# Optimization experiments

Measured on AMD Instinct MI355X. Metric: run time of the kernel, lower is better.

The kernel has to match this reference:

```python
import jax, jax.numpy as jnp
import numpy as np

B, L, HID = 4, 4096, 1024
H, D = 16, 64  # num_heads, head_dim


def setup_inputs() -> dict:
    key = jax.random.key(0)
    ks = jax.random.split(key, 5)
    s = 1.0 / np.sqrt(HID)
    mk = lambda k: jax.random.uniform(k, (HID, HID), minval=-s, maxval=s, dtype=jnp.float32)
    return {
        "x": jax.random.normal(ks[0], (B, L, HID), dtype=jnp.float32),
        "Wq": mk(ks[1]), "bq": jnp.zeros((HID,), jnp.float32),
        "Wk": mk(ks[2]), "bk": jnp.zeros((HID,), jnp.float32),
        "Wv": mk(ks[3]), "bv": jnp.zeros((HID,), jnp.float32),
        "Wo": mk(ks[4]), "bo": jnp.zeros((HID,), jnp.float32),
    }


def reference(x, Wq, bq, Wk, bk, Wv, bv, Wo, bo):
    Bx, Lx, _ = x.shape
    # projections (weights stored [in, out])
    q = (x @ Wq + bq).reshape(Bx, Lx, H, D)
    k = (x @ Wk + bk).reshape(Bx, Lx, H, D)
    v = (x @ Wv + bv).reshape(Bx, Lx, H, D)
    # Single window (L <= window_size): torch matmul batches over (B, L) and
    # contracts head_dim -> per-token head-to-head scores [B, L, H, H].
    scores = jnp.einsum('blhd,bled->blhe', q, k) / np.sqrt(D).astype(np.float32)
    probs = jax.nn.softmax(scores, axis=-1)
    out = jnp.einsum('blhe,bled->blhd', probs, v).reshape(Bx, Lx, HID)
    return out @ Wo + bo
```

## Files before the change

kernel.cpp:

```cpp
#include <hip/hip_runtime.h>
#include <stdint.h>


typedef __attribute__((ext_vector_type(8))) short short8;
typedef __attribute__((ext_vector_type(4))) float floatx4;
typedef __attribute__((address_space(1))) unsigned int gu32;
typedef __attribute__((address_space(3))) unsigned int lu32;

#define HID 1024
#define MTOK 16384
#define WELEM (HID * HID)
#define XELEM (MTOK * HID)

#define SBAR() __builtin_amdgcn_s_barrier()
#define WAITLGKM() do { asm volatile("s_waitcnt lgkmcnt(0)" ::: "memory"); \
                        __builtin_amdgcn_sched_barrier(0); } while (0)

__device__ __forceinline__ unsigned short f2bf(float f) {
  union { float f; uint32_t u; } v; v.f = f;
  uint32_t u = v.u;
  u += 0x7fffu + ((u >> 16) & 1u);
  return (unsigned short)(u >> 16);
}

__global__ __launch_bounds__(256) void cvt_x_kernel(const float* __restrict__ x,
                                                    unsigned short* __restrict__ xb) {
  const int idx = blockIdx.x * 256 + threadIdx.x;
  float4 v = ((const float4*)x)[idx];
  ushort4 o;
  o.x = f2bf(v.x); o.y = f2bf(v.y); o.z = f2bf(v.z); o.w = f2bf(v.w);
  ((ushort4*)xb)[idx] = o;
}

__global__ __launch_bounds__(256) void cvt_w_kernel(const float* __restrict__ W0,
                                                    const float* __restrict__ W1,
                                                    const float* __restrict__ W2,
                                                    const float* __restrict__ W3,
                                                    unsigned short* __restrict__ WT) {
  const float* W = (blockIdx.z == 0) ? W0 : (blockIdx.z == 1) ? W1
                   : (blockIdx.z == 2) ? W2 : W3;
  unsigned short* out = WT + (size_t)blockIdx.z * WELEM;
  __shared__ float tile[64][65];
  const int t = threadIdx.x;
  const int n0 = blockIdx.x * 64, k0 = blockIdx.y * 64;
#pragma unroll
  for (int i = 0; i < 4; i++) {
    const int row = i * 16 + (t >> 4);
    const int col = (t & 15) * 4;
    float4 v = *(const float4*)&W[(size_t)(k0 + row) * HID + n0 + col];
    tile[row][col] = v.x; tile[row][col + 1] = v.y;
    tile[row][col + 2] = v.z; tile[row][col + 3] = v.w;
  }
  __syncthreads();
#pragma unroll
  for (int i = 0; i < 4; i++) {
    const int n = i * 16 + (t >> 4);
    const int k = (t & 15) * 4;
    ushort4 o;
    o.x = f2bf(tile[k][n]);     o.y = f2bf(tile[k + 1][n]);
    o.z = f2bf(tile[k + 2][n]); o.w = f2bf(tile[k + 3][n]);
    *(ushort4*)&out[(size_t)(n0 + n) * HID + k0 + k] = o;
  }
}

template <bool QKV>
__global__ __launch_bounds__(512, 2) void gemm256(
    const unsigned short* __restrict__ A,
    const unsigned short* __restrict__ BTb,
    const float* __restrict__ b0, const float* __restrict__ b1,
    const float* __restrict__ b2,
    void* __restrict__ Cv)
{
  __shared__ short8 smem_[131072 / 16];
  char* smem = (char*)smem_;

  const int bid = blockIdx.x;
  const int xcd = bid & 7;
  const int j = bid >> 3;
  const int nb = j >> 3;
  const int mb = xcd * 8 + (j & 7);
  const int m0 = mb * 256;
  const int n0 = nb * 256;

  const unsigned short* BT = QKV ? BTb : (BTb + (size_t)3 * WELEM);

  const int t_ = threadIdx.x;
  const int wv = t_ >> 6, lane = t_ & 63;
  const int quad = lane >> 4, r16 = lane & 15;
  const int wm = wv >> 2, wn = wv & 3;

  const int srow = wv * 16 + (lane >> 2);
  const int scol = ((lane & 3) ^ ((lane >> 3) & 3)) * 8;
  const unsigned short* Ag = A  + (size_t)(m0 + srow) * HID + scol;
  const unsigned short* Bg = BT + (size_t)(n0 + srow) * HID + scol;

  const int qsw = (quad ^ ((r16 >> 1) & 3)) << 4;
  const char* Ard = smem + wm * 16384 + r16 * 64 + qsw;
  const char* Brd = smem + 32768 + (wn >> 1) * 16384 + ((wn & 1) * 64 + r16) * 64 + qsw;

  floatx4 acc[8][4] = {};

  auto stageA = [&](int h, int tt) {
    const unsigned short* s = Ag + (size_t)h * 128 * HID + tt * 64;
    char* d = smem + ((tt & 1) << 16) + h * 16384 + wv * 1024;
    __builtin_amdgcn_global_load_lds((const gu32*)s,        (lu32*)d,          16, 0, 0);
    __builtin_amdgcn_global_load_lds((const gu32*)(s + 32), (lu32*)(d + 8192), 16, 0, 0);
  };
  auto stageB = [&](int h, int tt) {
    const unsigned short* s = Bg + (size_t)h * 128 * HID + tt * 64;
    char* d = smem + ((tt & 1) << 16) + 32768 + h * 16384 + wv * 1024;
    __builtin_amdgcn_global_load_lds((const gu32*)s,        (lu32*)d,          16, 0, 0);
    __builtin_amdgcn_global_load_lds((const gu32*)(s + 32), (lu32*)(d + 8192), 16, 0, 0);
  };

  stageA(0, 0); stageA(1, 0); stageB(0, 0); stageB(1, 0);
  stageB(0, 1); stageA(0, 1);
  asm volatile("s_waitcnt vmcnt(4)" ::: "memory");
  SBAR();

  short8 a[4][2], b01[2][2], b23[2][2];
  const int NT = HID / 64;

  for (int t = 0; t < NT; ++t) {
    const int bufb = (t & 1) << 16;

#pragma unroll
    for (int ks = 0; ks < 2; ++ks) {
#pragma unroll
      for (int mi = 0; mi < 4; ++mi)
        a[mi][ks] = *(const short8*)(Ard + bufb + ks * 8192 + mi * 1024);
#pragma unroll
      for (int ni = 0; ni < 2; ++ni)
        b01[ni][ks] = *(const short8*)(Brd + bufb + ks * 8192 + ni * 1024);
    }
    if (t + 1 < NT) stageA(1, t + 1);
    SBAR(); WAITLGKM();
    __builtin_amdgcn_s_setprio(1);
#pragma unroll
    for (int ks = 0; ks < 2; ++ks)
#pragma unroll
      for (int mi = 0; mi < 4; ++mi)
#pragma unroll
        for (int ni = 0; ni < 2; ++ni)
          acc[mi][ni] = __builtin_amdgcn_mfma_f32_16x16x32_bf16(a[mi][ks], b01[ni][ks], acc[mi][ni], 0, 0, 0);
    __builtin_amdgcn_s_setprio(0);
    SBAR();

#pragma unroll
    for (int ks = 0; ks < 2; ++ks)
#pragma unroll
      for (int ni = 0; ni < 2; ++ni)
        b23[ni][ks] = *(const short8*)(Brd + bufb + ks * 8192 + (2 + ni) * 1024);
    if (t + 1 < NT) stageB(1, t + 1);
    SBAR(); WAITLGKM();
    __builtin_amdgcn_s_setprio(1);
#pragma unroll
    for (int ks = 0; ks < 2; ++ks)
#pragma unroll
      for (int mi = 0; mi < 4; ++mi)
#pragma unroll
        for (int ni = 0; ni < 2; ++ni)
          acc[mi][2 + ni] = __builtin_amdgcn_mfma_f32_16x16x32_bf16(a[mi][ks], b23[ni][ks], acc[mi][2 + ni], 0, 0, 0);
    __builtin_amdgcn_s_setprio(0);
    SBAR();

#pragma unroll
    for (int ks = 0; ks < 2; ++ks) {
#pragma unroll
      for (int mi = 0; mi < 4; ++mi)
        a[mi][ks] = *(const short8*)(Ard + bufb + ks * 8192 + (4 + mi) * 1024);
#pragma unroll
      for (int ni = 0; ni < 2; ++ni)
        b01[ni][ks] = *(const short8*)(Brd + bufb + ks * 8192 + ni * 1024);
    }
    SBAR(); WAITLGKM();
    __builtin_amdgcn_s_setprio(1);
#pragma unroll
    for (int ks = 0; ks < 2; ++ks)
#pragma unroll
      for (int mi = 0; mi < 4; ++mi)
#pragma unroll
        for (int ni = 0; ni < 2; ++ni)
          acc[4 + mi][ni] = __builtin_amdgcn_mfma_f32_16x16x32_bf16(a[mi][ks], b01[ni][ks], acc[4 + mi][ni], 0, 0, 0);
    __builtin_amdgcn_s_setprio(0);
    SBAR();

    if (t + 2 < NT) { stageB(0, t + 2); stageA(0, t + 2); }
    SBAR();
    __builtin_amdgcn_s_setprio(1);
#pragma unroll
    for (int ks = 0; ks < 2; ++ks)
#pragma unroll
      for (int mi = 0; mi < 4; ++mi)
#pragma unroll
        for (int ni = 0; ni < 2; ++ni)
          acc[4 + mi][2 + ni] = __builtin_amdgcn_mfma_f32_16x16x32_bf16(a[mi][ks], b23[ni][ks], acc[4 + mi][2 + ni], 0, 0, 0);
    __builtin_amdgcn_s_setprio(0);
    if (t + 2 < NT)      { asm volatile("s_waitcnt vmcnt(4)" ::: "memory"); }
    else if (t + 1 < NT) { asm volatile("s_waitcnt vmcnt(0)" ::: "memory"); }
    SBAR();
  }

  const int cb = QKV ? (n0 & 1023) : n0;
  const int zX = QKV ? (n0 >> 10) : 0;
  const float* bias = QKV ? ((zX == 0) ? b0 : ((zX == 1) ? b1 : b2)) : b0;

  float bvv[4];
#pragma unroll
  for (int ni = 0; ni < 4; ++ni) bvv[ni] = bias[cb + wn * 64 + ni * 16 + r16];

  const int row0 = m0 + wm * 128 + quad * 4;
  unsigned short* outb = (unsigned short*)Cv + (size_t)zX * XELEM;
  float* outf = (float*)Cv;
#pragma unroll
  for (int mi = 0; mi < 8; ++mi) {
#pragma unroll
    for (int rr = 0; rr < 4; ++rr) {
      const size_t roff = (size_t)(row0 + mi * 16 + rr) * HID + cb + wn * 64 + r16;
#pragma unroll
      for (int ni = 0; ni < 4; ++ni) {
        const float val = acc[mi][ni][rr] + bvv[ni];
        if constexpr (QKV) outb[roff + ni * 16] = f2bf(val);
        else               outf[roff + ni * 16] = val;
      }
    }
  }
}

__global__ __launch_bounds__(256) void attn_kernel(const unsigned short* qkv,
                                                   unsigned short* attn) {
  __shared__ unsigned short vls[4][1056];
  __shared__ unsigned short pls[4][16 * 24];

  const int t = threadIdx.x;
  const int wv = t >> 6, lane = t & 63;
  const int quad = lane >> 4, r16 = lane & 15;
  const size_t base = ((size_t)blockIdx.x * 4 + wv) * HID;
  const unsigned short* qp = qkv + base;
  const unsigned short* kp = qkv + (size_t)XELEM + base;
  const unsigned short* vp = qkv + 2 * (size_t)XELEM + base;

  __builtin_amdgcn_global_load_lds((const gu32*)(vp + lane * 8),       (lu32*)&vls[wv][0],   16, 0, 0);
  __builtin_amdgcn_global_load_lds((const gu32*)(vp + 512 + lane * 8), (lu32*)&vls[wv][528], 16, 0, 0);

  short8 qf0 = *(const short8*)(qp + r16 * 64 + quad * 8);
  short8 qf1 = *(const short8*)(qp + r16 * 64 + quad * 8 + 32);
  short8 kf0 = *(const short8*)(kp + r16 * 64 + quad * 8);
  short8 kf1 = *(const short8*)(kp + r16 * 64 + quad * 8 + 32);

  floatx4 sc = {0.f, 0.f, 0.f, 0.f};
  sc = __builtin_amdgcn_mfma_f32_16x16x32_bf16(qf0, kf0, sc, 0, 0, 0);
  sc = __builtin_amdgcn_mfma_f32_16x16x32_bf16(qf1, kf1, sc, 0, 0, 0);

#pragma unroll
  for (int rr = 0; rr < 4; rr++) {
    float s = sc[rr] * 0.125f;
    float m = s;
#pragma unroll
    for (int off = 1; off < 16; off <<= 1) m = fmaxf(m, __shfl_xor(m, off));
    float ex = __expf(s - m);
    float sum = ex;
#pragma unroll
    for (int off = 1; off < 16; off <<= 1) sum += __shfl_xor(sum, off);
    pls[wv][(quad * 4 + rr) * 24 + r16] = f2bf(ex / sum);
  }

  __syncthreads();

  const short8 zero8 = {0, 0, 0, 0, 0, 0, 0, 0};
  short8 af = zero8;
  short8 bf[4] = {zero8, zero8, zero8, zero8};
  if (quad < 2) {
    af = *(const short8*)&pls[wv][r16 * 24 + quad * 8];
#pragma unroll
    for (int c = 0; c < 4; c++)
#pragma unroll
      for (int jj = 0; jj < 8; jj++)
        bf[c][jj] = (short)vls[wv][quad * 528 + jj * 64 + c * 16 + r16];
  }

  floatx4 ov[4];
#pragma unroll
  for (int c = 0; c < 4; c++) {
    floatx4 z = {0.f, 0.f, 0.f, 0.f};
    ov[c] = __builtin_amdgcn_mfma_f32_16x16x32_bf16(af, bf[c], z, 0, 0, 0);
  }

#pragma unroll
  for (int rr = 0; rr < 4; rr++)
#pragma unroll
    for (int c = 0; c < 4; c++)
      attn[base + (size_t)(quad * 4 + rr) * 64 + c * 16 + r16] = f2bf(ov[c][rr]);
}

extern "C" void kernel_launch(void* const* d_in, const int* in_sizes, int n_in,
                              void* d_out, int out_size, void* d_ws, size_t ws_size,
                              hipStream_t stream) {
  const float* x  = (const float*)d_in[0];
  const float* Wq = (const float*)d_in[1];
  const float* bq = (const float*)d_in[2];
  const float* Wk = (const float*)d_in[3];
  const float* bk = (const float*)d_in[4];
  const float* Wv = (const float*)d_in[5];
  const float* bv = (const float*)d_in[6];
  const float* Wo = (const float*)d_in[7];
  const float* bo = (const float*)d_in[8];

  char* ws = (char*)d_ws;
  unsigned short* xb  = (unsigned short*)ws;
  unsigned short* wt  = (unsigned short*)(ws + (size_t)XELEM * 2);
  unsigned short* qkv = wt + 4 * (size_t)WELEM;

  cvt_x_kernel<<<XELEM / 1024, 256, 0, stream>>>(x, xb);
  cvt_w_kernel<<<dim3(16, 16, 4), 256, 0, stream>>>(Wq, Wk, Wv, Wo, wt);
  gemm256<true><<<768, 512, 0, stream>>>(xb, wt, bq, bk, bv, (void*)qkv);
  attn_kernel<<<4096, 256, 0, stream>>>(qkv, qkv);
  gemm256<false><<<256, 512, 0, stream>>>(qkv, wt, bo, bo, bo, d_out);
}
```

Baseline: 302.5 us.

## Loop each QKV GEMM block over Q,K,V weights and pipeline B-fragment reads across tiles

The QKV GEMM now launches 256 blocks, each computing the same 256x256 output tile for all three projections in sequence. A block reloads the next weight's first tiles while it writes out the current epilogue. Inside the K loop, the B-fragment registers for columns 0-1 are double-buffered, so the next tile's fragments are read during the current tile. The stage ordering and vmcnt waits are reworked to match. This trims LDS reads and hides latency at the cost of more registers. It also drops the grid from 768 to 256 blocks, which cuts parallelism and may leave CUs underused.

```diff
diff --git a/kernel.cpp b/kernel.cpp
--- a/kernel.cpp
+++ b/kernel.cpp
@@ -15,6 +15,8 @@
 #define SBAR() __builtin_amdgcn_s_barrier()
 #define WAITLGKM() do { asm volatile("s_waitcnt lgkmcnt(0)" ::: "memory"); \
                         __builtin_amdgcn_sched_barrier(0); } while (0)
+#define VMCNT(n) do { asm volatile("s_waitcnt vmcnt(" #n ")" ::: "memory"); \
+                      __builtin_amdgcn_sched_barrier(0); } while (0)
 
 __device__ __forceinline__ unsigned short f2bf(float f) {
   union { float f; uint32_t u; } v; v.f = f;
@@ -74,15 +76,16 @@
   __shared__ short8 smem_[131072 / 16];
   char* smem = (char*)smem_;
 
+  constexpr int R = QKV ? 3 : 1;
   const int bid = blockIdx.x;
   const int xcd = bid & 7;
   const int j = bid >> 3;
-  const int nb = j >> 3;
+  const int nb0 = j >> 3;
   const int mb = xcd * 8 + (j & 7);
   const int m0 = mb * 256;
-  const int n0 = nb * 256;
-
-  const unsigned short* BT = QKV ? BTb : (BTb + (size_t)3 * WELEM);
+  const int cb = nb0 * 256;
+
+  const unsigned short* BT0 = QKV ? BTb : (BTb + (size_t)3 * WELEM);
 
   const int t_ = threadIdx.x;
   const int wv = t_ >> 6, lane = t_ & 63;
@@ -91,8 +94,8 @@
 
   const int srow = wv * 16 + (lane >> 2);
   const int scol = ((lane & 3) ^ ((lane >> 3) & 3)) * 8;
-  const unsigned short* Ag = A  + (size_t)(m0 + srow) * HID + scol;
-  const unsigned short* Bg = BT + (size_t)(n0 + srow) * HID + scol;
+  const unsigned short* Ag = A + (size_t)(m0 + srow) * HID + scol;
+  const unsigned short* Bg = BT0 + (size_t)(cb + srow) * HID + scol;
 
   const int qsw = (quad ^ ((r16 >> 1) & 3)) << 4;
   const char* Ard = smem + wm * 16384 + r16 * 64 + qsw;
@@ -113,26 +116,36 @@
     __builtin_amdgcn_global_load_lds((const gu32*)(s + 32), (lu32*)(d + 8192), 16, 0, 0);
   };
 
-  stageA(0, 0); stageA(1, 0); stageB(0, 0); stageB(1, 0);
-  stageB(0, 1); stageA(0, 1);
-  asm volatile("s_waitcnt vmcnt(4)" ::: "memory");
-  SBAR();
-
-  short8 a[4][2], b01[2][2], b23[2][2];
   const int NT = HID / 64;
 
-  for (int t = 0; t < NT; ++t) {
-    const int bufb = (t & 1) << 16;
-
-#pragma unroll
-    for (int ks = 0; ks < 2; ++ks) {
+  short8 a[4][2];
+  short8 b23[2][2];
+  short8 bA[2][2], bB[2][2];
+
+  auto TILE = [&](int t, int bufb, int othb, short8 (&bc)[2][2], short8 (&bn)[2][2]) {
+#pragma unroll
+    for (int ks = 0; ks < 2; ++ks)
 #pragma unroll
       for (int mi = 0; mi < 4; ++mi)
         a[mi][ks] = *(const short8*)(Ard + bufb + ks * 8192 + mi * 1024);
+    if (t + 1 < NT) stageA(0, t + 1);
+    SBAR(); WAITLGKM();
+    __builtin_amdgcn_s_setprio(1);
+#pragma unroll
+    for (int ks = 0; ks < 2; ++ks)
+#pragma unroll
+      for (int mi = 0; mi < 4; ++mi)
+#pragma unroll
+        for (int ni = 0; ni < 2; ++ni)
+          acc[mi][ni] = __builtin_amdgcn_mfma_f32_16x16x32_bf16(a[mi][ks], bc[ni][ks], acc[mi][ni], 0, 0, 0);
+    __builtin_amdgcn_s_setprio(0);
+    SBAR();
+
+#pragma unroll
+    for (int ks = 0; ks < 2; ++ks)
 #pragma unroll
       for (int ni = 0; ni < 2; ++ni)
-        b01[ni][ks] = *(const short8*)(Brd + bufb + ks * 8192 + ni * 1024);
-    }
+        b23[ni][ks] = *(const short8*)(Brd + bufb + ks * 8192 + (2 + ni) * 1024);
     if (t + 1 < NT) stageA(1, t + 1);
     SBAR(); WAITLGKM();
     __builtin_amdgcn_s_setprio(1);
@@ -142,16 +155,16 @@
       for (int mi = 0; mi < 4; ++mi)
 #pragma unroll
         for (int ni = 0; ni < 2; ++ni)
-          acc[mi][ni] = __builtin_amdgcn_mfma_f32_16x16x32_bf16(a[mi][ks], b01[ni][ks], acc[mi][ni], 0, 0, 0);
+          acc[mi][2 + ni] = __builtin_amdgcn_mfma_f32_16x16x32_bf16(a[mi][ks], b23[ni][ks], acc[mi][2 + ni], 0, 0, 0);
     __builtin_amdgcn_s_setprio(0);
     SBAR();
 
 #pragma unroll
     for (int ks = 0; ks < 2; ++ks)
 #pragma unroll
-      for (int ni = 0; ni < 2; ++ni)
-        b23[ni][ks] = *(const short8*)(Brd + bufb + ks * 8192 + (2 + ni) * 1024);
-    if (t + 1 < NT) stageB(1, t + 1);
+      for (int mi = 0; mi < 4; ++mi)
+        a[mi][ks] = *(const short8*)(Ard + bufb + ks * 8192 + (4 + mi) * 1024);
+    if (t + 2 < NT) stageB(0, t + 2);
     SBAR(); WAITLGKM();
     __builtin_amdgcn_s_setprio(1);
 #pragma unroll
@@ -160,69 +173,94 @@
       for (int mi = 0; mi < 4; ++mi)
 #pragma unroll
         for (int ni = 0; ni < 2; ++ni)
-          acc[mi][2 + ni] = __builtin_amdgcn_mfma_f32_16x16x32_bf16(a[mi][ks], b23[ni][ks], acc[mi][2 + ni], 0, 0, 0);
-    __builtin_amdgcn_s_setprio(0);
-    SBAR();
-
-#pragma unroll
-    for (int ks = 0; ks < 2; ++ks) {
-#pragma unroll
-      for (int mi = 0; mi < 4; ++mi)
-        a[mi][ks] = *(const short8*)(Ard + bufb + ks * 8192 + (4 + mi) * 1024);
-#pragma unroll
-      for (int ni = 0; ni < 2; ++ni)
-        b01[ni][ks] = *(const short8*)(Brd + bufb + ks * 8192 + ni * 1024);
-    }
-    SBAR(); WAITLGKM();
-    __builtin_amdgcn_s_setprio(1);
-#pragma unroll
-    for (int ks = 0; ks < 2; ++ks)
-#pragma unroll
-      for (int mi = 0; mi < 4; ++mi)
-#pragma unroll
-        for (int ni = 0; ni < 2; ++ni)
-          acc[4 + mi][ni] = __builtin_amdgcn_mfma_f32_16x16x32_bf16(a[mi][ks], b01[ni][ks], acc[4 + mi][ni], 0, 0, 0);
-    __builtin_amdgcn_s_setprio(0);
-    SBAR();
-
-    if (t + 2 < NT) { stageB(0, t + 2); stageA(0, t + 2); }
-    SBAR();
-    __builtin_amdgcn_s_setprio(1);
-#pragma unroll
-    for (int ks = 0; ks < 2; ++ks)
-#pragma unroll
-      for (int mi = 0; mi < 4; ++mi)
-#pragma unroll
-        for (int ni = 0; ni < 2; ++ni)
           acc[4 + mi][2 + ni] = __builtin_amdgcn_mfma_f32_16x16x32_bf16(a[mi][ks], b23[ni][ks], acc[4 + mi][2 + ni], 0, 0, 0);
     __builtin_amdgcn_s_setprio(0);
-    if (t + 2 < NT)      { asm volatile("s_waitcnt vmcnt(4)" ::: "memory"); }
-    else if (t + 1 < NT) { asm volatile("s_waitcnt vmcnt(0)" ::: "memory"); }
-    SBAR();
-  }
-
-  const int cb = QKV ? (n0 & 1023) : n0;
-  const int zX = QKV ? (n0 >> 10) : 0;
-  const float* bias = QKV ? ((zX == 0) ? b0 : ((zX == 1) ? b1 : b2)) : b0;
-
-  float bvv[4];
-#pragma unroll
-  for (int ni = 0; ni < 4; ++ni) bvv[ni] = bias[cb + wn * 64 + ni * 16 + r16];
-
-  const int row0 = m0 + wm * 128 + quad * 4;
-  unsigned short* outb = (unsigned short*)Cv + (size_t)zX * XELEM;
-  float* outf = (float*)Cv;
-#pragma unroll
-  for (int mi = 0; mi < 8; ++mi) {
-#pragma unroll
-    for (int rr = 0; rr < 4; ++rr) {
-      const size_t roff = (size_t)(row0 + mi * 16 + rr) * HID + cb + wn * 64 + r16;
-#pragma unroll
-      for (int ni = 0; ni < 4; ++ni) {
-        const float val = acc[mi][ni][rr] + bvv[ni];
-        if constexpr (QKV) outb[roff + ni * 16] = f2bf(val);
-        else               outf[roff + ni * 16] = val;
+    if (t + 2 < NT)      { VMCNT(6); }
+    else if (t + 1 < NT) { VMCNT(4); }
+    SBAR();
+
+    if (t + 1 < NT) {
+#pragma unroll
+      for (int ks = 0; ks < 2; ++ks)
+#pragma unroll
+        for (int ni = 0; ni < 2; ++ni)
+          bn[ni][ks] = *(const short8*)(Brd + othb + ks * 8192 + ni * 1024);
+    }
+    if (t + 2 < NT) stageB(1, t + 2);
+    SBAR();
+    __builtin_amdgcn_s_setprio(1);
+#pragma unroll
+    for (int ks = 0; ks < 2; ++ks)
+#pragma unroll
+      for (int mi = 0; mi < 4; ++mi)
+#pragma unroll
+        for (int ni = 0; ni < 2; ++ni)
+          acc[4 + mi][ni] = __builtin_amdgcn_mfma_f32_16x16x32_bf16(a[mi][ks], bc[ni][ks], acc[4 + mi][ni], 0, 0, 0);
+    __builtin_amdgcn_s_setprio(0);
+    if (t + 2 < NT)      { VMCNT(4); }
+    else if (t + 1 < NT) { VMCNT(0); }
+    SBAR();
+  };
+
+  stageA(0, 0); stageA(1, 0); stageB(0, 0); stageB(1, 0);
+  stageB(0, 1); stageB(1, 1);
+  VMCNT(4);
+  SBAR();
+#pragma unroll
+  for (int ks = 0; ks < 2; ++ks)
+#pragma unroll
+    for (int ni = 0; ni < 2; ++ni)
+      bA[ni][ks] = *(const short8*)(Brd + ks * 8192 + ni * 1024);
+
+  for (int r = 0; r < R; ++r) {
+    for (int t = 0; t < NT; t += 2) {
+      TILE(t,     0,       0x10000, bA, bB);
+      TILE(t + 1, 0x10000, 0,       bB, bA);
+    }
+
+    if (r + 1 < R) {
+      Bg += WELEM;
+      stageA(0, 0); stageA(1, 0); stageB(0, 0); stageB(1, 0);
+      stageB(0, 1); stageB(1, 1);
+    }
+
+    {
+      const float* bias = QKV ? ((r == 0) ? b0 : ((r == 1) ? b1 : b2)) : b0;
+      float bvv[4];
+#pragma unroll
+      for (int ni = 0; ni < 4; ++ni) bvv[ni] = bias[cb + wn * 64 + ni * 16 + r16];
+
+      const int row0 = m0 + wm * 128 + quad * 4;
+      unsigned short* outb = (unsigned short*)Cv + (size_t)r * XELEM;
+      float* outf = (float*)Cv;
+#pragma unroll
+      for (int mi = 0; mi < 8; ++mi) {
+#pragma unroll
+        for (int rr = 0; rr < 4; ++rr) {
+          const size_t roff = (size_t)(row0 + mi * 16 + rr) * HID + cb + wn * 64 + r16;
+#pragma unroll
+          for (int ni = 0; ni < 4; ++ni) {
+            const float val = acc[mi][ni][rr] + bvv[ni];
+            if constexpr (QKV) outb[roff + ni * 16] = f2bf(val);
+            else               outf[roff + ni * 16] = val;
+          }
+        }
       }
+    }
+
+    if (r + 1 < R) {
+#pragma unroll
+      for (int mi = 0; mi < 8; ++mi)
+#pragma unroll
+        for (int ni = 0; ni < 4; ++ni)
+          acc[mi][ni] = floatx4{0.f, 0.f, 0.f, 0.f};
+      VMCNT(0);
+      SBAR();
+#pragma unroll
+      for (int ks = 0; ks < 2; ++ks)
+#pragma unroll
+        for (int ni = 0; ni < 2; ++ni)
+          bA[ni][ks] = *(const short8*)(Brd + ks * 8192 + ni * 1024);
     }
   }
 }
@@ -313,7 +351,7 @@
 
   cvt_x_kernel<<<XELEM / 1024, 256, 0, stream>>>(x, xb);
   cvt_w_kernel<<<dim3(16, 16, 4), 256, 0, stream>>>(Wq, Wk, Wv, Wo, wt);
-  gemm256<true><<<768, 512, 0, stream>>>(xb, wt, bq, bk, bv, (void*)qkv);
+  gemm256<true><<<256, 512, 0, stream>>>(xb, wt, bq, bk, bv, (void*)qkv);
   attn_kernel<<<4096, 256, 0, stream>>>(qkv, qkv);
   gemm256<false><<<256, 512, 0, stream>>>(qkv, wt, bo, bo, bo, d_out);
 }
```

Measured after the change: 292.6 us. 3.3% less time.
